# Performance work log

Measured on AMD Instinct MI355X. Metric: run time of the kernel, lower is better.

Reference implementation:

```python
import jax, jax.numpy as jnp
import numpy as np

B, S, D, H, DK, DV = 2, 2048, 1024, 16, 64, 64


def setup_inputs() -> dict:
    key = jax.random.key(0)
    ks = jax.random.split(key, 12)
    inp = {
        "query": jax.random.normal(ks[0], (B, S, D), jnp.float32),
        "key":   jax.random.normal(ks[1], (B, S, D), jnp.float32),
        "value": jax.random.normal(ks[2], (B, S, D), jnp.float32),
        # additive mask broadcast over per-head [B,S,S] scores (zeros = no masking)
        "mask":  jnp.zeros((S, S), jnp.float32),
        # stacked per-head projection params (math-equivalent to H separate Linears)
        "Wq": jax.random.normal(ks[3], (H, D, DK), jnp.float32) / np.sqrt(D),
        "bq": jax.random.normal(ks[4], (H, DK), jnp.float32) * 0.02,
        "Wk": jax.random.normal(ks[5], (H, D, DK), jnp.float32) / np.sqrt(D),
        "bk": jax.random.normal(ks[6], (H, DK), jnp.float32) * 0.02,
        "Wv": jax.random.normal(ks[7], (H, D, DV), jnp.float32) / np.sqrt(D),
        "bv": jax.random.normal(ks[8], (H, DV), jnp.float32) * 0.02,
        "Wo": jax.random.normal(ks[9], (H * DV, D), jnp.float32) / np.sqrt(H * DV),
        "bo": jax.random.normal(ks[10], (D,), jnp.float32) * 0.02,
    }
    return inp


def reference(query, key, value, mask, Wq, bq, Wk, bk, Wv, bv, Wo, bo):
    # per-head projections, vectorized over heads
    q = jnp.einsum("bsd,hdk->bhsk", query, Wq) + bq[None, :, None, :]
    k = jnp.einsum("bsd,hdk->bhsk", key, Wk) + bk[None, :, None, :]
    v = jnp.einsum("bsd,hdv->bhsv", value, Wv) + bv[None, :, None, :]
    # explicit QK^T softmax V, scale by sqrt(dim_k) (key.size(-1))
    scores = jnp.einsum("bhsk,bhtk->bhst", q, k) / jnp.sqrt(jnp.asarray(DK, q.dtype))
    scores = scores + mask  # broadcast [S,S] -> [B,H,S,S]
    attn = jax.nn.softmax(scores, axis=-1)
    out = jnp.einsum("bhst,bhtv->bhsv", attn, v)
    # concat heads along last dim: [B,S,H*DV]
    out = out.transpose(0, 2, 1, 3).reshape(B, S, H * DV)
    return out @ Wo + bo
```

## Files before the change

### kernel.cpp

```cpp
#include <hip/hip_runtime.h>
#include <stdint.h>

typedef __bf16 bf16;
typedef float f32x4 __attribute__((ext_vector_type(4)));
typedef __bf16 bf16x8 __attribute__((ext_vector_type(8)));
typedef __bf16 bf16x4 __attribute__((ext_vector_type(4)));
typedef __bf16 bf16x2 __attribute__((ext_vector_type(2)));
typedef unsigned u32x2 __attribute__((ext_vector_type(2)));
typedef unsigned u32x4 __attribute__((ext_vector_type(4)));

__device__ __forceinline__ void async_load16(const void* g, void* l) {
    __builtin_amdgcn_global_load_lds(
        (const __attribute__((address_space(1))) void*)g,
        (__attribute__((address_space(3))) void*)l, 16, 0, 0);
}

__device__ __forceinline__ unsigned pk2(float lo, float hi) {
    bf16x2 t;
    t[0] = (bf16)lo;
    t[1] = (bf16)hi;
    return __builtin_bit_cast(unsigned, t);
}

#if __has_builtin(__builtin_amdgcn_permlane32_swap)
#define PLSWAP32(A_, B_) do { u32x2 _r = __builtin_amdgcn_permlane32_swap((A_), (B_), false, false); (A_) = _r[0]; (B_) = _r[1]; } while (0)
#else
#define PLSWAP32(A_, B_) asm("v_permlane32_swap_b32 %0, %1" : "+v"(A_), "+v"(B_))
#endif
#if __has_builtin(__builtin_amdgcn_permlane16_swap)
#define PLSWAP16(A_, B_) do { u32x2 _r = __builtin_amdgcn_permlane16_swap((A_), (B_), false, false); (A_) = _r[0]; (B_) = _r[1]; } while (0)
#else
#define PLSWAP16(A_, B_) asm("v_permlane16_swap_b32 %0, %1" : "+v"(A_), "+v"(B_))
#endif

__global__ void detect_dtype(const unsigned short* __restrict__ q, int* __restrict__ flag) {
    __shared__ int cnt;
    if (threadIdx.x == 0) cnt = 0;
    __syncthreads();
    int c = 0;
    for (int i = threadIdx.x; i < 4096; i += 256) {
        int e = (q[i] >> 7) & 0xFF;
        if (e >= 0xC0) ++c;
    }
    atomicAdd(&cnt, c);
    __syncthreads();
    if (threadIdx.x == 0) { flag[0] = (cnt > 64) ? 1 : 0; flag[1] = 0; }
}

__global__ void prep(const void* __restrict__ qv, const void* __restrict__ vv,
                     const void* __restrict__ wq, const void* __restrict__ wk,
                     const void* __restrict__ wv, const void* __restrict__ wo,
                     const unsigned int* __restrict__ mask,
                     bf16* __restrict__ Xq, bf16* __restrict__ Xv,
                     bf16* __restrict__ WqT, bf16* __restrict__ WoT,
                     int* __restrict__ flag) {
    __shared__ bf16 t[32][33];
    const int f    = flag[0];
    const int task = blockIdx.z;
    const int bid  = blockIdx.x + 64 * blockIdx.y;

    if (task < 2) {
        const void* x = task ? vv : qv;
        bf16* o = task ? Xv : Xq;
        size_t i = ((size_t)bid * 256 + threadIdx.x) * 8;
        if (f) {
            f32x4 a = ((const f32x4*)x)[i / 4];
            f32x4 b = ((const f32x4*)x)[i / 4 + 1];
            bf16x8 v;
            for (int j = 0; j < 4; ++j) { v[j] = (bf16)a[j]; v[4 + j] = (bf16)b[j]; }
            *(bf16x8*)(o + i) = v;
        } else {
            *(bf16x8*)(o + i) = *(const bf16x8*)((const bf16*)x + i);
        }
    } else if (task < 5) {
        if (bid >= 1024) return;
        const void* in = (task == 2) ? wq : ((task == 3) ? wk : wv);
        int sub = bid >> 6, rem = bid & 63;
        int c0 = (rem & 1) * 32, r0 = (rem >> 1) * 32;
        int tx = threadIdx.x & 31, ty = threadIdx.x >> 5;
        size_t base = (size_t)sub * 65536;
        if (f) {
            const float* inF = (const float*)in;
            for (int i = 0; i < 32; i += 8)
                t[ty + i][tx] = (bf16)inF[base + (size_t)(r0 + ty + i) * 64 + (c0 + tx)];
        } else {
            const bf16* inB = (const bf16*)in;
            for (int i = 0; i < 32; i += 8)
                t[ty + i][tx] = inB[base + (size_t)(r0 + ty + i) * 64 + (c0 + tx)];
        }
        __syncthreads();
        bf16* o = WqT + ((size_t)(task - 2) * 16 + sub) * 65536;
        for (int i = 0; i < 32; i += 8)
            o[(size_t)(c0 + ty + i) * 1024 + (r0 + tx)] = t[tx][ty + i];
    } else if (task == 5) {
        if (bid >= 1024) return;
        int c0 = (bid & 31) * 32, r0 = (bid >> 5) * 32;
        int tx = threadIdx.x & 31, ty = threadIdx.x >> 5;
        if (f) {
            const float* inF = (const float*)wo;
            for (int i = 0; i < 32; i += 8)
                t[ty + i][tx] = (bf16)inF[(size_t)(r0 + ty + i) * 1024 + (c0 + tx)];
        } else {
            const bf16* inB = (const bf16*)wo;
            for (int i = 0; i < 32; i += 8)
                t[ty + i][tx] = inB[(size_t)(r0 + ty + i) * 1024 + (c0 + tx)];
        }
        __syncthreads();
        for (int i = 0; i < 32; i += 8)
            WoT[(size_t)(c0 + ty + i) * 1024 + (r0 + tx)] = t[tx][ty + i];
    } else {
        const long nvec = (f ? 4194304L : 2097152L) / 4;
        unsigned int acc = 0;
        long stride = 2048L * 256;
        for (long i = (long)bid * 256 + threadIdx.x; i < nvec; i += stride) {
            uint4 v = ((const uint4*)mask)[i];
            acc |= v.x | v.y | v.z | v.w;
        }
        if (acc) atomicOr(flag + 1, 1);
    }
}

__global__ __launch_bounds__(256, 3) void gemm_qkv(
    const bf16* __restrict__ Xq, const void* __restrict__ keyRaw,
    const bf16* __restrict__ Xv, const bf16* __restrict__ Bt,
    const void* __restrict__ b0, const void* __restrict__ b1, const void* __restrict__ b2,
    bf16* __restrict__ Qp, bf16* __restrict__ Kp, bf16* __restrict__ Vt,
    const int* __restrict__ flag) {
    __shared__ __attribute__((aligned(16))) unsigned char AsRaw[128 * 64 * 4];
    __shared__ __attribute__((aligned(16))) bf16 Bs[128 * 64];

    const int f = flag[0];
    const int K = 1024, N = 1024;
    const int z = blockIdx.z;
    const int af = (z == 1) ? f : 0;
    const void* Av   = (z == 0) ? (const void*)Xq : ((z == 1) ? keyRaw : (const void*)Xv);
    const void* bias = (z == 0) ? b0 : ((z == 1) ? b1 : b2);
    const bf16* B    = Bt + (size_t)z * 1024 * 1024;

    const int tid  = threadIdx.x;
    const int lane = tid & 63;
    const int w    = tid >> 6;
    const int quad = lane >> 4;
    const int mrow = lane & 15;
    const int m0 = blockIdx.y * 128;
    const int n0 = blockIdx.x * 128;
    const int wm = (w & 1) * 64;
    const int wn = (w >> 1) * 64;

    f32x4 acc[4][4] = {};

    for (int k0 = 0; k0 < K; k0 += 64) {
        if (af) {
            for (int it = 0; it < 8; ++it) {
                int ci  = it * 256 + tid;
                int row = ci >> 4, pc = ci & 15;
                int swz = ((row & 7) << 1) | ((row >> 3) & 1);
                int gc  = pc ^ swz;
                async_load16((const float*)Av + (size_t)(m0 + row) * K + k0 + gc * 4,
                             AsRaw + (size_t)(it * 256 + w * 64) * 16);
            }
        } else {
            for (int it = 0; it < 4; ++it) {
                int ci  = it * 256 + tid;
                int row = ci >> 3, pc = ci & 7;
                int gc  = pc ^ (row & 7);
                async_load16((const bf16*)Av + (size_t)(m0 + row) * K + k0 + gc * 8,
                             (bf16*)AsRaw + (size_t)(it * 256 + w * 64) * 8);
            }
        }
        for (int it = 0; it < 4; ++it) {
            int ci  = it * 256 + tid;
            int row = ci >> 3, pc = ci & 7;
            int gc  = pc ^ (row & 7);
            async_load16(B + (size_t)(n0 + row) * K + k0 + gc * 8,
                         Bs + (size_t)(it * 256 + w * 64) * 8);
        }
        __syncthreads();
        for (int kk = 0; kk < 2; ++kk) {
            bf16x8 afr[4], bfr[4];
            if (af) {
                const float* Asf = (const float*)AsRaw;
                for (int mi = 0; mi < 4; ++mi) {
                    int row = wm + mi * 16 + mrow;
                    int swz = ((row & 7) << 1) | ((row >> 3) & 1);
                    int lc  = (kk * 4 + quad) * 2;
                    f32x4 u0 = *(const f32x4*)(Asf + row * 64 + (lc ^ swz) * 4);
                    f32x4 u1 = *(const f32x4*)(Asf + row * 64 + ((lc + 1) ^ swz) * 4);
                    for (int j = 0; j < 4; ++j) {
                        afr[mi][j]     = (bf16)u0[j];
                        afr[mi][4 + j] = (bf16)u1[j];
                    }
                }
            } else {
                const bf16* Asb = (const bf16*)AsRaw;
                for (int mi = 0; mi < 4; ++mi) {
                    int row = wm + mi * 16 + mrow;
                    int pc  = (kk * 4 + quad) ^ (row & 7);
                    afr[mi] = *(const bf16x8*)(Asb + row * 64 + pc * 8);
                }
            }
            for (int ni = 0; ni < 4; ++ni) {
                int row = wn + ni * 16 + mrow;
                int pc  = (kk * 4 + quad) ^ (row & 7);
                bfr[ni] = *(const bf16x8*)(Bs + row * 64 + pc * 8);
            }
            for (int mi = 0; mi < 4; ++mi)
                for (int ni = 0; ni < 4; ++ni)
                    acc[mi][ni] = __builtin_amdgcn_mfma_f32_16x16x32_bf16(
                        afr[mi], bfr[ni], acc[mi][ni], 0, 0, 0);
        }
        __syncthreads();
    }

    const float scl = (z == 0) ? 0.18033688f : 1.0f;
    for (int ni = 0; ni < 4; ++ni) {
        int n    = n0 + wn + ni * 16 + mrow;
        float bv = f ? ((const float*)bias)[n] : (float)((const bf16*)bias)[n];
        for (int mi = 0; mi < 4; ++mi) {
            int mb = m0 + wm + mi * 16 + quad * 4;
            if (z == 2) {
                bf16x4 pk;
                for (int r = 0; r < 4; ++r) pk[r] = (bf16)(acc[mi][ni][r] + bv);
                *(bf16x4*)(Vt + (((size_t)(mb >> 11) * 1024 + n) << 11) + (mb & 2047)) = pk;
            } else {
                bf16* P = (z == 0) ? Qp : Kp;
                for (int r = 0; r < 4; ++r)
                    P[(size_t)(mb + r) * N + n] = (bf16)((acc[mi][ni][r] + bv) * scl);
            }
        }
    }
}

__global__ __launch_bounds__(256, 2) void gemm_out(
    const bf16* __restrict__ A, const bf16* __restrict__ Bt,
    const void* __restrict__ bias, void* __restrict__ Cout,
    const int* __restrict__ flag) {
    __shared__ __attribute__((aligned(16))) bf16 As[128 * 64];
    __shared__ __attribute__((aligned(16))) bf16 Bs[64 * 64];

    const int f = flag[0];
    const int K = 1024, N = 1024;
    const int tid  = threadIdx.x;
    const int lane = tid & 63;
    const int w    = tid >> 6;
    const int quad = lane >> 4;
    const int mrow = lane & 15;
    const int m0 = blockIdx.y * 128;
    const int n0 = blockIdx.x * 64;
    const int wm = (w & 1) * 64;
    const int wn = (w >> 1) * 32;

    f32x4 acc[4][2] = {};

    for (int k0 = 0; k0 < K; k0 += 64) {
        for (int it = 0; it < 4; ++it) {
            int ci  = it * 256 + tid;
            int row = ci >> 3, pc = ci & 7;
            int gc  = pc ^ (row & 7);
            async_load16(A + (size_t)(m0 + row) * K + k0 + gc * 8,
                         As + (size_t)(it * 256 + w * 64) * 8);
        }
        for (int it = 0; it < 2; ++it) {
            int ci  = it * 256 + tid;
            int row = ci >> 3, pc = ci & 7;
            int gc  = pc ^ (row & 7);
            async_load16(Bt + (size_t)(n0 + row) * K + k0 + gc * 8,
                         Bs + (size_t)(it * 256 + w * 64) * 8);
        }
        __syncthreads();
        for (int kk = 0; kk < 2; ++kk) {
            bf16x8 afr[4], bfr[2];
            for (int mi = 0; mi < 4; ++mi) {
                int row = wm + mi * 16 + mrow;
                int pc  = (kk * 4 + quad) ^ (row & 7);
                afr[mi] = *(const bf16x8*)(As + row * 64 + pc * 8);
            }
            for (int ni = 0; ni < 2; ++ni) {
                int row = wn + ni * 16 + mrow;
                int pc  = (kk * 4 + quad) ^ (row & 7);
                bfr[ni] = *(const bf16x8*)(Bs + row * 64 + pc * 8);
            }
            for (int mi = 0; mi < 4; ++mi)
                for (int ni = 0; ni < 2; ++ni)
                    acc[mi][ni] = __builtin_amdgcn_mfma_f32_16x16x32_bf16(
                        afr[mi], bfr[ni], acc[mi][ni], 0, 0, 0);
        }
        __syncthreads();
    }

    for (int ni = 0; ni < 2; ++ni) {
        int n    = n0 + wn + ni * 16 + mrow;
        float bv = f ? ((const float*)bias)[n] : (float)((const bf16*)bias)[n];
        for (int mi = 0; mi < 4; ++mi) {
            int mb = m0 + wm + mi * 16 + quad * 4;
            for (int r = 0; r < 4; ++r) {
                float val = acc[mi][ni][r] + bv;
                if (f) ((float*)Cout)[(size_t)(mb + r) * N + n] = val;
                else   ((bf16*)Cout)[(size_t)(mb + r) * N + n] = (bf16)val;
            }
        }
    }
}

__global__ __launch_bounds__(512, 4) void flash_attn(
    const bf16* __restrict__ Qp, const bf16* __restrict__ Kp,
    const bf16* __restrict__ Vt, const void* __restrict__ maskv,
    bf16* __restrict__ O, const int* __restrict__ flag) {
    __shared__ __attribute__((aligned(16))) bf16 Ks[2][4096];
    __shared__ __attribute__((aligned(16))) bf16 Vs[2][4096];

    const int f       = flag[0];
    const int useMask = flag[1];
    const int tid  = threadIdx.x;
    const int lane = tid & 63;
    const int w    = tid >> 6;
    const int quad = lane >> 4;
    const int c    = lane & 15;

    const int flat = blockIdx.x + 16 * (blockIdx.y + 16 * blockIdx.z);
    const int rx   = flat & 7;
    const int sx   = flat >> 3;
    const int pair = rx + 8 * (sx >> 4);
    const int s0   = (sx & 15) * 128;
    const int h    = pair & 15;
    const int b    = pair >> 4;

    const size_t qkBase = (size_t)b * 2048 * 1024 + h * 64;
    const size_t vtBase = ((size_t)b * 1024 + h * 64) * 2048;

    const int r0 = tid >> 3, g0 = (tid & 7) ^ (r0 & 7);
    const bf16* kp0 = Kp + qkBase + (size_t)r0 * 1024 + g0 * 8;
    const bf16* vp0 = Vt + vtBase + (size_t)r0 * 2048 + g0 * 8;

#define STAGE(B_, T_) do {                                                      \
        async_load16(kp0 + (size_t)(T_) * 1024, &Ks[B_][(size_t)(w * 64) * 8]); \
        async_load16(vp0 + (T_),                &Vs[B_][(size_t)(w * 64) * 8]); \
    } while (0)

    const bf16* kf0 = &Ks[0][c * 64 + ((0 + quad) ^ (c & 7)) * 8];
    const bf16* kf1 = &Ks[0][c * 64 + ((4 + quad) ^ (c & 7)) * 8];
    const bf16* vf0 = &Vs[0][c * 64 + ((0 + quad) ^ (c & 7)) * 8];
    const bf16* vf1 = &Vs[0][c * 64 + ((4 + quad) ^ (c & 7)) * 8];

    const bf16* qrow = Qp + qkBase + (size_t)(s0 + w * 16 + c) * 1024;
    bf16x8 aq0 = *(const bf16x8*)(qrow + quad * 8);
    bf16x8 aq1 = *(const bf16x8*)(qrow + 32 + quad * 8);

    f32x4 o_acc[4] = {};
    float l_s = 0.f;

    const size_t mb0 = (size_t)(s0 + w * 16 + c) * 2048;

#define FCOMP(IB_, T_) do {                                                              \
        f32x4 sc[4] = {};                                                                \
        _Pragma("unroll") for (int tt = 0; tt < 4; ++tt) {                               \
            bf16x8 ak0 = *(const bf16x8*)(kf0 + (IB_) * 4096 + tt * 1024);               \
            bf16x8 ak1 = *(const bf16x8*)(kf1 + (IB_) * 4096 + tt * 1024);               \
            sc[tt] = __builtin_amdgcn_mfma_f32_16x16x32_bf16(ak0, aq0, sc[tt], 0, 0, 0); \
            sc[tt] = __builtin_amdgcn_mfma_f32_16x16x32_bf16(ak1, aq1, sc[tt], 0, 0, 0); \
        }                                                                                \
        if (useMask) {                                                                   \
            const size_t mr = mb0 + (T_);                                                \
            _Pragma("unroll") for (int tt = 0; tt < 4; ++tt) {                           \
                if (f) {                                                                 \
                    f32x4 mk = *(const f32x4*)((const float*)maskv + mr + tt * 16 + quad * 4); \
                    for (int r = 0; r < 4; ++r) sc[tt][r] += mk[r] * 1.44269504f;        \
                } else {                                                                 \
                    bf16x4 mk = *(const bf16x4*)((const bf16*)maskv + mr + tt * 16 + quad * 4); \
                    for (int r = 0; r < 4; ++r) sc[tt][r] += (float)mk[r] * 1.44269504f; \
                }                                                                        \
            }                                                                            \
        }                                                                                \
        unsigned Wp[4][2];                                                               \
        {                                                                                \
            float rsum = 0.f;                                                            \
            _Pragma("unroll") for (int tt = 0; tt < 4; ++tt) {                           \
                float p0 = exp2f(sc[tt][0]), p1 = exp2f(sc[tt][1]);                      \
                float p2 = exp2f(sc[tt][2]), p3 = exp2f(sc[tt][3]);                      \
                rsum += (p0 + p1) + (p2 + p3);                                           \
                Wp[tt][0] = pk2(p0, p1);                                                 \
                Wp[tt][1] = pk2(p2, p3);                                                 \
            }                                                                            \
            l_s += rsum;                                                                 \
        }                                                                                \
        _Pragma("unroll") for (int kk = 0; kk < 2; ++kk) {                               \
            unsigned a0 = Wp[2 * kk][0], b0v = Wp[2 * kk + 1][0];                        \
            unsigned a1 = Wp[2 * kk][1], b1v = Wp[2 * kk + 1][1];                        \
            PLSWAP32(a0, b0v);                                                           \
            PLSWAP16(a0, b0v);                                                           \
            PLSWAP32(a1, b1v);                                                           \
            PLSWAP16(a1, b1v);                                                           \
            u32x4 uv; uv[0] = a0; uv[1] = a1; uv[2] = b0v; uv[3] = b1v;                  \
            bf16x8 ap = __builtin_bit_cast(bf16x8, uv);                                  \
            const bf16* vfb = kk ? vf1 : vf0;                                            \
            _Pragma("unroll") for (int ni = 0; ni < 4; ++ni) {                           \
                bf16x8 bv = *(const bf16x8*)(vfb + (IB_) * 4096 + ni * 1024);            \
                o_acc[ni] = __builtin_amdgcn_mfma_f32_16x16x32_bf16(ap, bv, o_acc[ni], 0, 0, 0); \
            }                                                                            \
        }                                                                                \
    } while (0)

    STAGE(0, 0);
    for (int t0 = 0; t0 < 2048; t0 += 128) {
        __syncthreads();
        STAGE(1, t0 + 64);
        FCOMP(0, t0);
        __syncthreads();
        if (t0 + 128 < 2048) STAGE(0, t0 + 128);
        FCOMP(1, t0 + 64);
    }
#undef STAGE
#undef FCOMP

    {
        float ls = l_s;
        ls += __shfl_xor(ls, 16, 64);
        ls += __shfl_xor(ls, 32, 64);
        for (int r = 0; r < 4; ++r) {
            float lv   = __shfl(ls, quad * 4 + r, 64);
            float inv  = 1.0f / lv;
            size_t roff = (size_t)(b * 2048 + s0 + w * 16 + quad * 4 + r) * 1024 + h * 64;
            for (int ni = 0; ni < 4; ++ni)
                O[roff + ni * 16 + c] = (bf16)(o_acc[ni][r] * inv);
        }
    }
}

extern "C" void kernel_launch(void* const* d_in, const int* in_sizes, int n_in,
                              void* d_out, int out_size, void* d_ws, size_t ws_size,
                              hipStream_t stream) {
    bf16* ws = (bf16*)d_ws;
    (void)in_sizes; (void)n_in; (void)out_size; (void)ws_size;

    const size_t MM = 1024 * 1024;
    int*  flag = (int*)ws;
    bf16* WqT  = ws + 8;
    bf16* WoT  = WqT + 3 * MM;
    bf16* Qp   = WoT + MM;
    bf16* Kp   = Qp + 4 * MM;
    bf16* Xq   = Kp + 4 * MM;
    bf16* AO   = Xq;
    bf16* Xv   = (bf16*)d_out;
    bf16* Vt   = (bf16*)d_out + 4 * MM;

    detect_dtype<<<1, 256, 0, stream>>>((const unsigned short*)d_in[0], flag);

    prep<<<dim3(64, 32, 7), 256, 0, stream>>>(d_in[0], d_in[2], d_in[4], d_in[6],
                                              d_in[8], d_in[10],
                                              (const unsigned int*)d_in[3],
                                              Xq, Xv, WqT, WoT, flag);

    gemm_qkv<<<dim3(8, 32, 3), 256, 0, stream>>>(Xq, d_in[1], Xv, WqT,
                                                 d_in[5], d_in[7], d_in[9],
                                                 Qp, Kp, Vt, flag);

    flash_attn<<<dim3(16, 16, 2), 512, 0, stream>>>(Qp, Kp, Vt, d_in[3], AO, flag);

    gemm_out<<<dim3(16, 32, 1), 256, 0, stream>>>(AO, WoT, d_in[11], d_out, flag);
}
```

Before: 262.5 us.

## Triple-buffer K/V tiles in flash attention with partial vmcnt waits

Moves the flash-attention K/V staging from a double buffer with two full barriers per 128-key step to a three-slot ring. Each 64-key step now waits only for the oldest outstanding async loads (vmcnt(2)) and uses a single barrier, so two tiles stay in flight while one is computed. The last iterations issue redundant wrap-around loads to keep the waitcnt pattern uniform. The cost is 50% more LDS per block, which may cut occupancy, plus reliance on hand-written waitcnt correctness.

```diff
diff --git a/kernel.cpp b/kernel.cpp
--- a/kernel.cpp
+++ b/kernel.cpp
@@ -306,8 +306,8 @@
     const bf16* __restrict__ Qp, const bf16* __restrict__ Kp,
     const bf16* __restrict__ Vt, const void* __restrict__ maskv,
     bf16* __restrict__ O, const int* __restrict__ flag) {
-    __shared__ __attribute__((aligned(16))) bf16 Ks[2][4096];
-    __shared__ __attribute__((aligned(16))) bf16 Vs[2][4096];
+    __shared__ __attribute__((aligned(16))) bf16 Ks[3][4096];
+    __shared__ __attribute__((aligned(16))) bf16 Vs[3][4096];
 
     const int f       = flag[0];
     const int useMask = flag[1];
@@ -351,11 +351,11 @@
 
     const size_t mb0 = (size_t)(s0 + w * 16 + c) * 2048;
 
-#define FCOMP(IB_, T_) do {                                                              \
+#define FCOMP(OFF_, T_) do {                                                             \
         f32x4 sc[4] = {};                                                                \
         _Pragma("unroll") for (int tt = 0; tt < 4; ++tt) {                               \
-            bf16x8 ak0 = *(const bf16x8*)(kf0 + (IB_) * 4096 + tt * 1024);               \
-            bf16x8 ak1 = *(const bf16x8*)(kf1 + (IB_) * 4096 + tt * 1024);               \
+            bf16x8 ak0 = *(const bf16x8*)(kf0 + (OFF_) + tt * 1024);                     \
+            bf16x8 ak1 = *(const bf16x8*)(kf1 + (OFF_) + tt * 1024);                     \
             sc[tt] = __builtin_amdgcn_mfma_f32_16x16x32_bf16(ak0, aq0, sc[tt], 0, 0, 0); \
             sc[tt] = __builtin_amdgcn_mfma_f32_16x16x32_bf16(ak1, aq1, sc[tt], 0, 0, 0); \
         }                                                                                \
@@ -392,23 +392,29 @@
             PLSWAP16(a1, b1v);                                                           \
             u32x4 uv; uv[0] = a0; uv[1] = a1; uv[2] = b0v; uv[3] = b1v;                  \
             bf16x8 ap = __builtin_bit_cast(bf16x8, uv);                                  \
-            const bf16* vfb = kk ? vf1 : vf0;                                            \
+            const bf16* vfb = (kk ? vf1 : vf0) + (OFF_);                                 \
             _Pragma("unroll") for (int ni = 0; ni < 4; ++ni) {                           \
-                bf16x8 bv = *(const bf16x8*)(vfb + (IB_) * 4096 + ni * 1024);            \
+                bf16x8 bv = *(const bf16x8*)(vfb + ni * 1024);                           \
                 o_acc[ni] = __builtin_amdgcn_mfma_f32_16x16x32_bf16(ap, bv, o_acc[ni], 0, 0, 0); \
             }                                                                            \
         }                                                                                \
     } while (0)
 
     STAGE(0, 0);
-    for (int t0 = 0; t0 < 2048; t0 += 128) {
-        __syncthreads();
-        STAGE(1, t0 + 64);
-        FCOMP(0, t0);
-        __syncthreads();
-        if (t0 + 128 < 2048) STAGE(0, t0 + 128);
-        FCOMP(1, t0 + 64);
-    }
+    STAGE(1, 64);
+    int cur = 0;
+    for (int t = 0; t < 32; ++t) {
+        asm volatile("s_waitcnt vmcnt(2)" ::: "memory");
+        __builtin_amdgcn_s_barrier();
+        __builtin_amdgcn_sched_barrier(0);
+        int nxt = cur + 2;
+        if (nxt >= 3) nxt -= 3;
+        STAGE(nxt, ((t + 2) & 31) * 64);
+        FCOMP(cur * 4096, t * 64);
+        ++cur;
+        if (cur == 3) cur = 0;
+    }
+    asm volatile("s_waitcnt vmcnt(0)" ::: "memory");
 #undef STAGE
 #undef FCOMP
 
```

Result: slower. 270.9 us (+3.2%).
